# Kernel tuning notes

Measured on AMD Instinct MI355X. Metric: run time of the kernel, lower is better.

## Reference

```python
import jax, jax.numpy as jnp
import numpy as np

N, K, D, E, H = 65536, 8, 256, 256, 132  # points, components, latent_dim, encoder_dim, FC hidden

def setup_inputs() -> dict:
    key = jax.random.key(0)
    ks = jax.random.split(key, 12)
    s = 0.05
    f32 = jnp.float32
    return {
        "signal": jax.random.normal(ks[0], (N, E), f32),
        "components": jax.random.normal(ks[1], (K, N, D), f32),
        # message_map / update_map: Linear(D, D)
        "Wm": jax.random.normal(ks[2], (D, D), f32) * s,
        "bm": jnp.zeros((D,), f32),
        "Wu": jax.random.normal(ks[3], (D, D), f32) * s,
        "bu": jnp.zeros((D,), f32),
        "W0": jax.random.normal(ks[4], (H, E + D), f32) * s,
        "b0": jnp.zeros((H,), f32),
        "W1": jax.random.normal(ks[5], (H, H), f32) * s,
        "b1": jnp.zeros((H,), f32),
        "W2": jax.random.normal(ks[6], (H, H), f32) * s,
        "b2": jnpes if False else jnp.zeros((H,), f32),
        "W3": jax.random.normal(ks[7], (D, H), f32) * s,
        "b3": jnp.zeros((D,), f32),
    }

def reference(signal, components, Wm, bm, Wu, bu, W0, b0, W1, b1, W2, b2, W3, b3):
    k = components.shape[0]
    # sum_k Linear(comp_k) == Linear applied to sum, with bias counted k times (linearity)
    right = components.sum(0) @ Wm.T + k * bm          # [N, D]
    right = right @ Wu.T + bu                          # update_map
    x = jnp.concatenate([signal, right], axis=-1)      # [N, E+D]
    x = jax.nn.relu(x @ W0.T + b0)
    x = jax.nn.relu(x @ W1.T + b1)
    x = jax.nn.relu(x @ W2.T + b2)
    return x @ W3.T + b3                               # [N, D]
```

## Files before the change

### kernel.cpp

```cpp
#include <hip/hip_runtime.h>
#include <hip/hip_bf16.h>


typedef float  f32x4  __attribute__((ext_vector_type(4)));
typedef __bf16 bf16x8 __attribute__((ext_vector_type(8)));
typedef unsigned int   u32x2 __attribute__((ext_vector_type(2)));
typedef unsigned short u16x8 __attribute__((ext_vector_type(8)));

__device__ __forceinline__ unsigned short f2bf(float f) {
  unsigned int u = __builtin_bit_cast(unsigned int, f);
  u += 0x7fffu + ((u >> 16) & 1u);
  return (unsigned short)(u >> 16);
}

__device__ __forceinline__ u32x2 pack4(f32x4 v) {
  u32x2 r;
  r[0] = (unsigned)f2bf(v[0]) | ((unsigned)f2bf(v[1]) << 16);
  r[1] = (unsigned)f2bf(v[2]) | ((unsigned)f2bf(v[3]) << 16);
  return r;
}

__global__ __launch_bounds__(256) void kP(
    const float* __restrict__ W0, const float* __restrict__ Wu,
    const float* __restrict__ Wm, const float* __restrict__ bm,
    const float* __restrict__ bu, const float* __restrict__ b0,
    const float* __restrict__ b1, const float* __restrict__ b2,
    float* __restrict__ Wc, float* __restrict__ bias1,
    float* __restrict__ b1p, float* __restrict__ b2p) {
  const int b = blockIdx.x;
  const int d = threadIdx.x;
  if (b < 132) {
    __shared__ float u[256];
    const int h = b;
    float s = 0.f;
#pragma unroll 8
    for (int i = 0; i < 256; ++i) s += W0[h * 512 + 256 + i] * Wu[i * 256 + d];
    u[d] = s;
    __syncthreads();
    float s2 = 0.f;
#pragma unroll 8
    for (int j = 0; j < 256; ++j) s2 += u[j] * Wm[j * 256 + d];
    Wc[h * 256 + d] = s2;
  } else {
    __shared__ float bml[256];
    __shared__ float rbl[256];
    bml[d] = bm[d];
    __syncthreads();
    {
      const f32x4* wr = (const f32x4*)(Wu + d * 256);
      const f32x4* bm4 = (const f32x4*)bml;
      float s = 0.f;
#pragma unroll 8
      for (int i = 0; i < 64; ++i) {
        f32x4 w = wr[i], v = bm4[i];
        s += w[0] * v[0] + w[1] * v[1] + w[2] * v[2] + w[3] * v[3];
      }
      rbl[d] = 8.f * s + bu[d];
    }
    __syncthreads();
    if (d < 160) {
      float v = 0.f;
      if (d < 132) {
        float s = 0.f;
#pragma unroll 8
        for (int j = 0; j < 256; ++j) s += W0[d * 512 + 256 + j] * rbl[j];
        v = b0[d] + s;
      }
      bias1[d] = v;
      b1p[d] = (d < 132) ? b1[d] : 0.f;
      b2p[d] = (d < 132) ? b2[d] : 0.f;
    }
  }
}

__global__ __launch_bounds__(256) void kC(
    const float* __restrict__ W0, const float* __restrict__ Wc,
    const float* __restrict__ W1, const float* __restrict__ W2,
    const float* __restrict__ W3,
    unsigned short* __restrict__ P1, unsigned short* __restrict__ P2,
    unsigned short* __restrict__ P3, unsigned short* __restrict__ P4) {
  int e = blockIdx.x * 256 + threadIdx.x;
  if (e >= 174080) return;
  unsigned short* dst; int NT, rel, mode;
  if (e < 81920)       { dst = P1; NT = 10; rel = e;          mode = 0; }
  else if (e < 107520) { dst = P2; NT = 10; rel = e - 81920;  mode = 1; }
  else if (e < 133120) { dst = P3; NT = 10; rel = e - 107520; mode = 2; }
  else                 { dst = P4; NT = 16; rel = e - 133120; mode = 3; }
  int chunk = rel >> 9, q = rel & 511;
  int lane = q >> 3, j = q & 7;
  int kk = chunk / NT, nt = chunk - kk * NT;
  int k = kk * 32 + (lane >> 4) * 8 + j;
  int n = nt * 16 + (lane & 15);
  float v = 0.f;
  if (mode == 0) {
    if (n < 132) v = (k < 256) ? W0[n * 512 + k] : Wc[n * 256 + (k - 256)];
  } else if (mode == 1) {
    if (n < 132 && k < 132) v = W1[n * 132 + k];
  } else if (mode == 2) {
    if (n < 132 && k < 132) v = W2[n * 132 + k];
  } else {
    if (k < 132) v = W3[n * 132 + k];
  }
  dst[rel] = f2bf(v);
}

#define WISS(BUF, CHUNK)                                                     \
  {                                                                          \
    _Pragma("unroll") for (int nt = 0; nt < 10; ++nt)                        \
        BUF[nt] = *(const bf16x8*)(Pb + (CHUNK) * 10240 + nt * 1024 +        \
                                   lane * 16);                               \
  }
#define WISS8(BUF, HALF)                                                     \
  {                                                                          \
    _Pragma("unroll") for (int nt = 0; nt < 8; ++nt)                         \
        BUF[nt] = *(const bf16x8*)(Pb + 266240 + (HALF) * 8192 + nt * 1024 + \
                                   lane * 16);                               \
  }
#define MFMA10(BUF)                                                          \
  {                                                                          \
    _Pragma("unroll") for (int nt = 0; nt < 10; ++nt)                        \
        acc[nt] = __builtin_amdgcn_mfma_f32_16x16x32_bf16(af, BUF[nt],       \
                                                          acc[nt], 0, 0, 0); \
  }

__global__ __launch_bounds__(256, 2) void kD(
    const float* __restrict__ signal, const float* __restrict__ comp,
    const unsigned short* __restrict__ Pseq,
    const float* __restrict__ bias1, const float* __restrict__ b1p,
    const float* __restrict__ b2p, const float* __restrict__ b3,
    float* __restrict__ out) {
  extern __shared__ char lds[];
  const int tid = threadIdx.x;
  const int wave = tid >> 6;
  const int lane = tid & 63;
  const int lhalf = lane >> 4;
  const int l16 = lane & 15;
  char* act = lds + wave * 8192;
  const char* Pb = (const char*)Pseq;
  const int row0 = ((int)blockIdx.x * 4 + wave) * 16;
  const int asw = (l16 & 7) << 4;
  const int r2 = lane >> 5, c32 = lane & 31;
  const f32x4* cp = (const f32x4*)comp;
  const size_t cbase = (size_t)(row0 + r2) * 64 + c32 * 2;

  f32x4 sg[16];
  const f32x4* sp = (const f32x4*)signal;
#pragma unroll
  for (int r = 0; r < 16; ++r) sg[r] = sp[(size_t)(row0 + r) * 64 + lane];

  bf16x8 wA[10], wB[10];
  WISS(wA, 0);

  f32x4 ct[4][2];
#pragma unroll
  for (int s = 0; s < 4; ++s) {
    ct[s][0] = cp[cbase + (size_t)s * 4194304u];
    ct[s][1] = cp[cbase + (size_t)s * 4194304u + 1];
  }

#pragma unroll
  for (int r = 0; r < 16; ++r)
    *(u32x2*)(act + r * 512 + ((lane * 8) ^ ((r & 7) << 4))) = pack4(sg[r]);

  f32x4 acc[10];
#pragma unroll
  for (int i = 0; i < 10; ++i) acc[i] = f32x4{0.f, 0.f, 0.f, 0.f};
  f32x4 ca0, ca1;
  u16x8 cs[8];

#pragma unroll
  for (int kk = 0; kk < 8; ++kk) {
    if (kk & 1) { WISS(wA, kk + 1); } else { WISS(wB, kk + 1); }
#pragma unroll
    for (int i = 0; i < 8; ++i) {
      const int s = kk * 8 + i;
      const int b4 = s & 3;
      if (i == 0) { ca0 = ct[b4][0]; ca1 = ct[b4][1]; }
      else        { ca0 += ct[b4][0]; ca1 += ct[b4][1]; }
      if (s + 4 < 64) {
        const int j2 = (s + 4) >> 3, k2 = (s + 4) & 7;
        ct[b4][0] = cp[cbase + (size_t)k2 * 4194304u + j2 * 128];
        ct[b4][1] = cp[cbase + (size_t)k2 * 4194304u + j2 * 128 + 1];
      }
    }
    {
      u16x8 v;
      v[0] = f2bf(ca0[0]); v[1] = f2bf(ca0[1]);
      v[2] = f2bf(ca0[2]); v[3] = f2bf(ca0[3]);
      v[4] = f2bf(ca1[0]); v[5] = f2bf(ca1[1]);
      v[6] = f2bf(ca1[2]); v[7] = f2bf(ca1[3]);
      cs[kk] = v;
    }
    bf16x8 af =
        *(const bf16x8*)(act + l16 * 512 + ((kk * 64 + lhalf * 16) ^ asw));
    if (kk & 1) { MFMA10(wB); } else { MFMA10(wA); }
  }

  asm volatile("" ::: "memory");
#pragma unroll
  for (int j = 0; j < 8; ++j) {
    const int rw = 2 * j + r2;
    *(u16x8*)(act + rw * 512 + ((c32 * 16) ^ ((rw & 7) << 4))) = cs[j];
  }
  asm volatile("" ::: "memory");

#pragma unroll
  for (int kk = 8; kk < 16; ++kk) {
    if (kk & 1) { WISS(wA, kk + 1); } else { WISS(wB, kk + 1); }
    bf16x8 af = *(const bf16x8*)(act + l16 * 512 +
                                 (((kk - 8) * 64 + lhalf * 16) ^ asw));
    if (kk & 1) { MFMA10(wB); } else { MFMA10(wA); }
  }

  {
    float bv[10];
#pragma unroll
    for (int nt = 0; nt < 10; ++nt) bv[nt] = bias1[nt * 16 + l16];
    asm volatile("" ::: "memory");
#pragma unroll
    for (int nt = 0; nt < 10; ++nt) {
#pragma unroll
      for (int r = 0; r < 4; ++r) {
        const int row = lhalf * 4 + r;
        float v = fmaxf(acc[nt][r] + bv[nt], 0.f);
        *(unsigned short*)(act + row * 512 +
                           (((nt * 16 + l16) * 2) ^ ((row & 7) << 4))) = f2bf(v);
      }
    }
    asm volatile("" ::: "memory");
  }

  bf16x8 w4A[8], w4B[8];
#pragma unroll
  for (int L = 0; L < 2; ++L) {
    const float* hbias = L ? b2p : b1p;
#pragma unroll
    for (int i = 0; i < 10; ++i) acc[i] = f32x4{0.f, 0.f, 0.f, 0.f};
#pragma unroll
    for (int q = 0; q < 5; ++q) {
      const int c = 16 + L * 5 + q;
      if (c < 25) {
        if (c & 1) { WISS(wA, c + 1); } else { WISS(wB, c + 1); }
      } else {
        WISS8(w4A, 0);
      }
      bf16x8 af =
          *(const bf16x8*)(act + l16 * 512 + ((q * 64 + lhalf * 16) ^ asw));
      if (c & 1) { MFMA10(wB); } else { MFMA10(wA); }
    }
    float bv[10];
#pragma unroll
    for (int nt = 0; nt < 10; ++nt) bv[nt] = hbias[nt * 16 + l16];
    asm volatile("" ::: "memory");
#pragma unroll
    for (int nt = 0; nt < 10; ++nt) {
#pragma unroll
      for (int r = 0; r < 4; ++r) {
        const int row = lhalf * 4 + r;
        float v = fmaxf(acc[nt][r] + bv[nt], 0.f);
        *(unsigned short*)(act + row * 512 +
                           (((nt * 16 + l16) * 2) ^ ((row & 7) << 4))) = f2bf(v);
      }
    }
    asm volatile("" ::: "memory");
  }

  f32x4 a4[16];
#pragma unroll
  for (int i = 0; i < 16; ++i) a4[i] = f32x4{0.f, 0.f, 0.f, 0.f};
#pragma unroll
  for (int h = 0; h < 10; ++h) {
    if (h < 9) {
      if (h & 1) { WISS8(w4A, h + 1); } else { WISS8(w4B, h + 1); }
    }
    bf16x8 af = *(const bf16x8*)(act + l16 * 512 +
                                 (((h >> 1) * 64 + lhalf * 16) ^ asw));
#pragma unroll
    for (int i = 0; i < 8; ++i) {
      const int nt = (h & 1) * 8 + i;
      if (h & 1)
        a4[nt] = __builtin_amdgcn_mfma_f32_16x16x32_bf16(af, w4B[i], a4[nt],
                                                         0, 0, 0);
      else
        a4[nt] = __builtin_amdgcn_mfma_f32_16x16x32_bf16(af, w4A[i], a4[nt],
                                                         0, 0, 0);
    }
  }

  float bv[16];
#pragma unroll
  for (int nt = 0; nt < 16; ++nt) bv[nt] = b3[nt * 16 + l16];
  float* op = out + (size_t)(row0 + lhalf * 4) * 256 + l16;
#pragma unroll
  for (int nt = 0; nt < 16; ++nt) {
#pragma unroll
    for (int r = 0; r < 4; ++r)
      op[(size_t)r * 256 + nt * 16] = a4[nt][r] + bv[nt];
  }
}

extern "C" void kernel_launch(void* const* d_in, const int* in_sizes, int n_in,
                              void* d_out, int out_size, void* d_ws, size_t ws_size,
                              hipStream_t stream) {
  const float* signal = (const float*)d_in[0];
  const float* comp   = (const float*)d_in[1];
  const float* Wm = (const float*)d_in[2];
  const float* bm = (const float*)d_in[3];
  const float* Wu = (const float*)d_in[4];
  const float* bu = (const float*)d_in[5];
  const float* W0 = (const float*)d_in[6];
  const float* b0 = (const float*)d_in[7];
  const float* W1 = (const float*)d_in[8];
  const float* b1 = (const float*)d_in[9];
  const float* W2 = (const float*)d_in[10];
  const float* b2 = (const float*)d_in[11];
  const float* W3 = (const float*)d_in[12];
  const float* b3 = (const float*)d_in[13];

  char* ws = (char*)d_ws;
  float* Wc    = (float*)(ws + 0);
  float* bias1 = (float*)(ws + 135168);
  float* b1p   = (float*)(ws + 135808);
  float* b2p   = (float*)(ws + 136448);
  unsigned short* P1 = (unsigned short*)(ws + 137216);
  unsigned short* P2 = (unsigned short*)(ws + 301056);
  unsigned short* P3 = (unsigned short*)(ws + 352256);
  unsigned short* P4 = (unsigned short*)(ws + 403456);

  hipLaunchKernelGGL(kP, dim3(133), dim3(256), 0, stream,
                     W0, Wu, Wm, bm, bu, b0, b1, b2, Wc, bias1, b1p, b2p);
  hipLaunchKernelGGL(kC, dim3(680), dim3(256), 0, stream,
                     W0, Wc, W1, W2, W3, P1, P2, P3, P4);
  hipLaunchKernelGGL(kD, dim3(1024), dim3(256), 32768, stream,
                     signal, comp, P1, bias1, b1p, b2p, b3, (float*)d_out);
}
```

Before: 201.4 us.

## Split kernel into producer blocks summing components and consumer MLP blocks with flags

The main kernel now launches 512 blocks. The first 256 blocks stream the components tensor, reduce over K, and write bf16 sums to workspace, then raise per-chunk flags with release atomics. The other 256 blocks each run the MLP over 4 chunks, spin-waiting on those flags before reading the precomputed sums. The aim is to separate the bandwidth-bound reduction from the MFMA work so both run concurrently on different CUs. In exchange it adds an extra write and read of the bf16 sums, and it can deadlock if consumer blocks take all the slots before producer blocks get scheduled.

Result: slower. 800.1 us (+297.3%).

```diff
diff --git a/kernel.cpp b/kernel.cpp
--- a/kernel.cpp
+++ b/kernel.cpp
@@ -26,7 +26,8 @@
     const float* __restrict__ bu, const float* __restrict__ b0,
     const float* __restrict__ b1, const float* __restrict__ b2,
     float* __restrict__ Wc, float* __restrict__ bias1,
-    float* __restrict__ b1p, float* __restrict__ b2p) {
+    float* __restrict__ b1p, float* __restrict__ b2p,
+    int* __restrict__ flags) {
   const int b = blockIdx.x;
   const int d = threadIdx.x;
   if (b < 132) {
@@ -42,6 +43,7 @@
     for (int j = 0; j < 256; ++j) s2 += u[j] * Wm[j * 256 + d];
     Wc[h * 256 + d] = s2;
   } else {
+    flags[d] = 0; flags[d + 256] = 0; flags[d + 512] = 0; flags[d + 768] = 0;
     __shared__ float bml[256];
     __shared__ float rbl[256];
     bml[d] = bm[d];
@@ -123,179 +125,200 @@
                                                           acc[nt], 0, 0, 0); \
   }
 
-__global__ __launch_bounds__(256, 2) void kD(
+__global__ __launch_bounds__(256, 2) void kMain(
     const float* __restrict__ signal, const float* __restrict__ comp,
     const unsigned short* __restrict__ Pseq,
     const float* __restrict__ bias1, const float* __restrict__ b1p,
     const float* __restrict__ b2p, const float* __restrict__ b3,
+    unsigned short* __restrict__ csum, int* flags,
     float* __restrict__ out) {
   extern __shared__ char lds[];
   const int tid = threadIdx.x;
-  const int wave = tid >> 6;
-  const int lane = tid & 63;
-  const int lhalf = lane >> 4;
-  const int l16 = lane & 15;
-  char* act = lds + wave * 8192;
-  const char* Pb = (const char*)Pseq;
-  const int row0 = ((int)blockIdx.x * 4 + wave) * 16;
-  const int asw = (l16 & 7) << 4;
-  const int r2 = lane >> 5, c32 = lane & 31;
-  const f32x4* cp = (const f32x4*)comp;
-  const size_t cbase = (size_t)(row0 + r2) * 64 + c32 * 2;
-
-  f32x4 sg[16];
-  const f32x4* sp = (const f32x4*)signal;
-#pragma unroll
-  for (int r = 0; r < 16; ++r) sg[r] = sp[(size_t)(row0 + r) * 64 + lane];
-
-  bf16x8 wA[10], wB[10];
-  WISS(wA, 0);
-
-  f32x4 ct[4][2];
-#pragma unroll
-  for (int s = 0; s < 4; ++s) {
-    ct[s][0] = cp[cbase + (size_t)s * 4194304u];
-    ct[s][1] = cp[cbase + (size_t)s * 4194304u + 1];
-  }
-
-#pragma unroll
-  for (int r = 0; r < 16; ++r)
-    *(u32x2*)(act + r * 512 + ((lane * 8) ^ ((r & 7) << 4))) = pack4(sg[r]);
-
-  f32x4 acc[10];
-#pragma unroll
-  for (int i = 0; i < 10; ++i) acc[i] = f32x4{0.f, 0.f, 0.f, 0.f};
-  f32x4 ca0, ca1;
-  u16x8 cs[8];
-
-#pragma unroll
-  for (int kk = 0; kk < 8; ++kk) {
-    if (kk & 1) { WISS(wA, kk + 1); } else { WISS(wB, kk + 1); }
-#pragma unroll
-    for (int i = 0; i < 8; ++i) {
-      const int s = kk * 8 + i;
-      const int b4 = s & 3;
-      if (i == 0) { ca0 = ct[b4][0]; ca1 = ct[b4][1]; }
-      else        { ca0 += ct[b4][0]; ca1 += ct[b4][1]; }
-      if (s + 4 < 64) {
-        const int j2 = (s + 4) >> 3, k2 = (s + 4) & 7;
-        ct[b4][0] = cp[cbase + (size_t)k2 * 4194304u + j2 * 128];
-        ct[b4][1] = cp[cbase + (size_t)k2 * 4194304u + j2 * 128 + 1];
+
+  if (blockIdx.x < 256) {
+    const int c = (int)blockIdx.x;
+    const f32x4* cp = (const f32x4*)comp;
+    u32x2* op = (u32x2*)csum;
+    for (int s = 0; s < 4; ++s) {
+      const size_t base = (size_t)(c * 16384 + s * 4096) + tid;
+      f32x4 a[16];
+#pragma unroll
+      for (int j = 0; j < 16; ++j) a[j] = cp[base + j * 256];
+#pragma unroll
+      for (int k = 1; k < 8; ++k) {
+        f32x4 t0[16];
+#pragma unroll
+        for (int j = 0; j < 16; ++j)
+          t0[j] = cp[base + (size_t)k * 4194304u + j * 256];
+#pragma unroll
+        for (int j = 0; j < 16; ++j) a[j] += t0[j];
+      }
+#pragma unroll
+      for (int j = 0; j < 16; ++j) op[base + j * 256] = pack4(a[j]);
+      __syncthreads();
+      if (tid == 0) {
+        __threadfence();
+        __hip_atomic_store(&flags[c * 4 + s], 1, __ATOMIC_RELEASE,
+                           __HIP_MEMORY_SCOPE_AGENT);
       }
     }
-    {
-      u16x8 v;
-      v[0] = f2bf(ca0[0]); v[1] = f2bf(ca0[1]);
-      v[2] = f2bf(ca0[2]); v[3] = f2bf(ca0[3]);
-      v[4] = f2bf(ca1[0]); v[5] = f2bf(ca1[1]);
-      v[6] = f2bf(ca1[2]); v[7] = f2bf(ca1[3]);
-      cs[kk] = v;
+  } else {
+    const int c = (int)blockIdx.x - 256;
+    const int wave = tid >> 6;
+    const int lane = tid & 63;
+    const int lhalf = lane >> 4;
+    const int l16 = lane & 15;
+    const int r2 = lane >> 5, c32 = lane & 31;
+    char* act = lds + wave * 8192;
+    const char* Pb = (const char*)Pseq;
+    const int asw = (l16 & 7) << 4;
+
+    for (int s = 0; s < 4; ++s) {
+      const int row0 = c * 256 + s * 64 + wave * 16;
+
+      {
+        f32x4 sg[16];
+        const f32x4* sp = (const f32x4*)signal;
+#pragma unroll
+        for (int r = 0; r < 16; ++r) sg[r] = sp[(size_t)(row0 + r) * 64 + lane];
+#pragma unroll
+        for (int r = 0; r < 16; ++r)
+          *(u32x2*)(act + r * 512 + ((lane * 8) ^ ((r & 7) << 4))) =
+              pack4(sg[r]);
+      }
+
+      bf16x8 wA[10], wB[10];
+      WISS(wA, 0);
+
+      {
+        const int fi = c * 4 + s;
+        while (__hip_atomic_load(&flags[fi], __ATOMIC_ACQUIRE,
+                                 __HIP_MEMORY_SCOPE_AGENT) == 0)
+          __builtin_amdgcn_s_sleep(16);
+      }
+
+      u16x8 cs[8];
+#pragma unroll
+      for (int j = 0; j < 8; ++j)
+        cs[j] = *(const u16x8*)(csum + (size_t)(row0 + 2 * j + r2) * 256 +
+                                c32 * 8);
+
+      f32x4 acc[10];
+#pragma unroll
+      for (int i = 0; i < 10; ++i) acc[i] = f32x4{0.f, 0.f, 0.f, 0.f};
+
+#pragma unroll
+      for (int kk = 0; kk < 8; ++kk) {
+        if (kk & 1) { WISS(wA, kk + 1); } else { WISS(wB, kk + 1); }
+        bf16x8 af =
+            *(const bf16x8*)(act + l16 * 512 + ((kk * 64 + lhalf * 16) ^ asw));
+        if (kk & 1) { MFMA10(wB); } else { MFMA10(wA); }
+      }
+
+      asm volatile("" ::: "memory");
+#pragma unroll
+      for (int j = 0; j < 8; ++j) {
+        const int rw = 2 * j + r2;
+        *(u16x8*)(act + rw * 512 + ((c32 * 16) ^ ((rw & 7) << 4))) = cs[j];
+      }
+      asm volatile("" ::: "memory");
+
+#pragma unroll
+      for (int kk = 8; kk < 16; ++kk) {
+        if (kk & 1) { WISS(wA, kk + 1); } else { WISS(wB, kk + 1); }
+        bf16x8 af = *(const bf16x8*)(act + l16 * 512 +
+                                     (((kk - 8) * 64 + lhalf * 16) ^ asw));
+        if (kk & 1) { MFMA10(wB); } else { MFMA10(wA); }
+      }
+
+      {
+        float bv[10];
+#pragma unroll
+        for (int nt = 0; nt < 10; ++nt) bv[nt] = bias1[nt * 16 + l16];
+        asm volatile("" ::: "memory");
+#pragma unroll
+        for (int nt = 0; nt < 10; ++nt) {
+#pragma unroll
+          for (int r = 0; r < 4; ++r) {
+            const int row = lhalf * 4 + r;
+            float v = fmaxf(acc[nt][r] + bv[nt], 0.f);
+            *(unsigned short*)(act + row * 512 +
+                               (((nt * 16 + l16) * 2) ^ ((row & 7) << 4))) =
+                f2bf(v);
+          }
+        }
+        asm volatile("" ::: "memory");
+      }
+
+      bf16x8 w4A[8], w4B[8];
+#pragma unroll
+      for (int L = 0; L < 2; ++L) {
+        const float* hbias = L ? b2p : b1p;
+#pragma unroll
+        for (int i = 0; i < 10; ++i) acc[i] = f32x4{0.f, 0.f, 0.f, 0.f};
+#pragma unroll
+        for (int q = 0; q < 5; ++q) {
+          const int cc = 16 + L * 5 + q;
+          if (cc < 25) {
+            if (cc & 1) { WISS(wA, cc + 1); } else { WISS(wB, cc + 1); }
+          } else {
+            WISS8(w4A, 0);
+          }
+          bf16x8 af =
+              *(const bf16x8*)(act + l16 * 512 + ((q * 64 + lhalf * 16) ^ asw));
+          if (cc & 1) { MFMA10(wB); } else { MFMA10(wA); }
+        }
+        float bv[10];
+#pragma unroll
+        for (int nt = 0; nt < 10; ++nt) bv[nt] = hbias[nt * 16 + l16];
+        asm volatile("" ::: "memory");
+#pragma unroll
+        for (int nt = 0; nt < 10; ++nt) {
+#pragma unroll
+          for (int r = 0; r < 4; ++r) {
+            const int row = lhalf * 4 + r;
+            float v = fmaxf(acc[nt][r] + bv[nt], 0.f);
+            *(unsigned short*)(act + row * 512 +
+                               (((nt * 16 + l16) * 2) ^ ((row & 7) << 4))) =
+                f2bf(v);
+          }
+        }
+        asm volatile("" ::: "memory");
+      }
+
+      f32x4 a4[16];
+#pragma unroll
+      for (int i = 0; i < 16; ++i) a4[i] = f32x4{0.f, 0.f, 0.f, 0.f};
+#pragma unroll
+      for (int h = 0; h < 10; ++h) {
+        if (h < 9) {
+          if (h & 1) { WISS8(w4A, h + 1); } else { WISS8(w4B, h + 1); }
+        }
+        bf16x8 af = *(const bf16x8*)(act + l16 * 512 +
+                                     (((h >> 1) * 64 + lhalf * 16) ^ asw));
+#pragma unroll
+        for (int i = 0; i < 8; ++i) {
+          const int nt = (h & 1) * 8 + i;
+          if (h & 1)
+            a4[nt] = __builtin_amdgcn_mfma_f32_16x16x32_bf16(af, w4B[i],
+                                                             a4[nt], 0, 0, 0);
+          else
+            a4[nt] = __builtin_amdgcn_mfma_f32_16x16x32_bf16(af, w4A[i],
+                                                             a4[nt], 0, 0, 0);
+        }
+      }
+
+      float bv[16];
+#pragma unroll
+      for (int nt = 0; nt < 16; ++nt) bv[nt] = b3[nt * 16 + l16];
+      float* op = out + (size_t)(row0 + lhalf * 4) * 256 + l16;
+#pragma unroll
+      for (int nt = 0; nt < 16; ++nt) {
+#pragma unroll
+        for (int r = 0; r < 4; ++r)
+          op[(size_t)r * 256 + nt * 16] = a4[nt][r] + bv[nt];
+      }
     }
-    bf16x8 af =
-        *(const bf16x8*)(act + l16 * 512 + ((kk * 64 + lhalf * 16) ^ asw));
-    if (kk & 1) { MFMA10(wB); } else { MFMA10(wA); }
-  }
-
-  asm volatile("" ::: "memory");
-#pragma unroll
-  for (int j = 0; j < 8; ++j) {
-    const int rw = 2 * j + r2;
-    *(u16x8*)(act + rw * 512 + ((c32 * 16) ^ ((rw & 7) << 4))) = cs[j];
-  }
-  asm volatile("" ::: "memory");
-
-#pragma unroll
-  for (int kk = 8; kk < 16; ++kk) {
-    if (kk & 1) { WISS(wA, kk + 1); } else { WISS(wB, kk + 1); }
-    bf16x8 af = *(const bf16x8*)(act + l16 * 512 +
-                                 (((kk - 8) * 64 + lhalf * 16) ^ asw));
-    if (kk & 1) { MFMA10(wB); } else { MFMA10(wA); }
-  }
-
-  {
-    float bv[10];
-#pragma unroll
-    for (int nt = 0; nt < 10; ++nt) bv[nt] = bias1[nt * 16 + l16];
-    asm volatile("" ::: "memory");
-#pragma unroll
-    for (int nt = 0; nt < 10; ++nt) {
-#pragma unroll
-      for (int r = 0; r < 4; ++r) {
-        const int row = lhalf * 4 + r;
-        float v = fmaxf(acc[nt][r] + bv[nt], 0.f);
-        *(unsigned short*)(act + row * 512 +
-                           (((nt * 16 + l16) * 2) ^ ((row & 7) << 4))) = f2bf(v);
-      }
-    }
-    asm volatile("" ::: "memory");
-  }
-
-  bf16x8 w4A[8], w4B[8];
-#pragma unroll
-  for (int L = 0; L < 2; ++L) {
-    const float* hbias = L ? b2p : b1p;
-#pragma unroll
-    for (int i = 0; i < 10; ++i) acc[i] = f32x4{0.f, 0.f, 0.f, 0.f};
-#pragma unroll
-    for (int q = 0; q < 5; ++q) {
-      const int c = 16 + L * 5 + q;
-      if (c < 25) {
-        if (c & 1) { WISS(wA, c + 1); } else { WISS(wB, c + 1); }
-      } else {
-        WISS8(w4A, 0);
-      }
-      bf16x8 af =
-          *(const bf16x8*)(act + l16 * 512 + ((q * 64 + lhalf * 16) ^ asw));
-      if (c & 1) { MFMA10(wB); } else { MFMA10(wA); }
-    }
-    float bv[10];
-#pragma unroll
-    for (int nt = 0; nt < 10; ++nt) bv[nt] = hbias[nt * 16 + l16];
-    asm volatile("" ::: "memory");
-#pragma unroll
-    for (int nt = 0; nt < 10; ++nt) {
-#pragma unroll
-      for (int r = 0; r < 4; ++r) {
-        const int row = lhalf * 4 + r;
-        float v = fmaxf(acc[nt][r] + bv[nt], 0.f);
-        *(unsigned short*)(act + row * 512 +
-                           (((nt * 16 + l16) * 2) ^ ((row & 7) << 4))) = f2bf(v);
-      }
-    }
-    asm volatile("" ::: "memory");
-  }
-
-  f32x4 a4[16];
-#pragma unroll
-  for (int i = 0; i < 16; ++i) a4[i] = f32x4{0.f, 0.f, 0.f, 0.f};
-#pragma unroll
-  for (int h = 0; h < 10; ++h) {
-    if (h < 9) {
-      if (h & 1) { WISS8(w4A, h + 1); } else { WISS8(w4B, h + 1); }
-    }
-    bf16x8 af = *(const bf16x8*)(act + l16 * 512 +
-                                 (((h >> 1) * 64 + lhalf * 16) ^ asw));
-#pragma unroll
-    for (int i = 0; i < 8; ++i) {
-      const int nt = (h & 1) * 8 + i;
-      if (h & 1)
-        a4[nt] = __builtin_amdgcn_mfma_f32_16x16x32_bf16(af, w4B[i], a4[nt],
-                                                         0, 0, 0);
-      else
-        a4[nt] = __builtin_amdgcn_mfma_f32_16x16x32_bf16(af, w4A[i], a4[nt],
-                                                         0, 0, 0);
-    }
-  }
-
-  float bv[16];
-#pragma unroll
-  for (int nt = 0; nt < 16; ++nt) bv[nt] = b3[nt * 16 + l16];
-  float* op = out + (size_t)(row0 + lhalf * 4) * 256 + l16;
-#pragma unroll
-  for (int nt = 0; nt < 16; ++nt) {
-#pragma unroll
-    for (int r = 0; r < 4; ++r)
-      op[(size_t)r * 256 + nt * 16] = a4[nt][r] + bv[nt];
   }
 }
 
@@ -326,11 +349,15 @@
   unsigned short* P2 = (unsigned short*)(ws + 301056);
   unsigned short* P3 = (unsigned short*)(ws + 352256);
   unsigned short* P4 = (unsigned short*)(ws + 403456);
+  int* flags = (int*)(ws + 485376);
+  unsigned short* csum = (unsigned short*)(ws + 489472);
 
   hipLaunchKernelGGL(kP, dim3(133), dim3(256), 0, stream,
-                     W0, Wu, Wm, bm, bu, b0, b1, b2, Wc, bias1, b1p, b2p);
+                     W0, Wu, Wm, bm, bu, b0, b1, b2, Wc, bias1, b1p, b2p,
+                     flags);
   hipLaunchKernelGGL(kC, dim3(680), dim3(256), 0, stream,
                      W0, Wc, W1, W2, W3, P1, P2, P3, P4);
-  hipLaunchKernelGGL(kD, dim3(1024), dim3(256), 32768, stream,
-                     signal, comp, P1, bias1, b1p, b2p, b3, (float*)d_out);
-}
+  hipLaunchKernelGGL(kMain, dim3(512), dim3(256), 32768, stream,
+                     signal, comp, P1, bias1, b1p, b2p, b3, csum, flags,
+                     (float*)d_out);
+}
```

## Feed first-layer MFMA directly from global loads without component pre-summing

Applied to the files above, without the earlier changes.

The first layer no longer sums the K components in registers and stages signal and summed components through LDS. Each lane now loads its MFMA A-fragment straight from global memory, converts it with the hardware packed bf16 convert instruction, and runs one MFMA per component chunk. This relies on the folded weight being the same for every component, so the summation happens inside the MFMA accumulation. That removes the LDS write/read round trip and the manual rounding code, but it multiplies first-layer MFMA work about 5x (72 instead of 16 k-steps) and issues smaller strided global loads.

Measured after the change: 273.0 us. +35.6%, slower.

```diff
diff --git a/kernel.cpp b/kernel.cpp
--- a/kernel.cpp
+++ b/kernel.cpp
@@ -4,8 +4,7 @@
 
 typedef float  f32x4  __attribute__((ext_vector_type(4)));
 typedef __bf16 bf16x8 __attribute__((ext_vector_type(8)));
-typedef unsigned int   u32x2 __attribute__((ext_vector_type(2)));
-typedef unsigned short u16x8 __attribute__((ext_vector_type(8)));
+typedef unsigned int   u32x4 __attribute__((ext_vector_type(4)));
 
 __device__ __forceinline__ unsigned short f2bf(float f) {
   unsigned int u = __builtin_bit_cast(unsigned int, f);
@@ -13,11 +12,14 @@
   return (unsigned short)(u >> 16);
 }
 
-__device__ __forceinline__ u32x2 pack4(f32x4 v) {
-  u32x2 r;
-  r[0] = (unsigned)f2bf(v[0]) | ((unsigned)f2bf(v[1]) << 16);
-  r[1] = (unsigned)f2bf(v[2]) | ((unsigned)f2bf(v[3]) << 16);
-  return r;
+__device__ __forceinline__ bf16x8 cvt8(f32x4 a, f32x4 b) {
+  unsigned r0, r1, r2, r3;
+  asm("v_cvt_pk_bf16_f32 %0, %1, %2" : "=v"(r0) : "v"(a[0]), "v"(a[1]));
+  asm("v_cvt_pk_bf16_f32 %0, %1, %2" : "=v"(r1) : "v"(a[2]), "v"(a[3]));
+  asm("v_cvt_pk_bf16_f32 %0, %1, %2" : "=v"(r2) : "v"(b[0]), "v"(b[1]));
+  asm("v_cvt_pk_bf16_f32 %0, %1, %2" : "=v"(r3) : "v"(b[2]), "v"(b[3]));
+  u32x4 r{r0, r1, r2, r3};
+  return __builtin_bit_cast(bf16x8, r);
 }
 
 __global__ __launch_bounds__(256) void kP(
@@ -139,77 +141,44 @@
   const char* Pb = (const char*)Pseq;
   const int row0 = ((int)blockIdx.x * 4 + wave) * 16;
   const int asw = (l16 & 7) << 4;
-  const int r2 = lane >> 5, c32 = lane & 31;
+
+  const f32x4* sp = (const f32x4*)signal;
   const f32x4* cp = (const f32x4*)comp;
-  const size_t cbase = (size_t)(row0 + r2) * 64 + c32 * 2;
-
-  f32x4 sg[16];
-  const f32x4* sp = (const f32x4*)signal;
-#pragma unroll
-  for (int r = 0; r < 16; ++r) sg[r] = sp[(size_t)(row0 + r) * 64 + lane];
+  const size_t abase = (size_t)(row0 + l16) * 64 + lhalf * 2;
 
   bf16x8 wA[10], wB[10];
   WISS(wA, 0);
 
-  f32x4 ct[4][2];
-#pragma unroll
-  for (int s = 0; s < 4; ++s) {
-    ct[s][0] = cp[cbase + (size_t)s * 4194304u];
-    ct[s][1] = cp[cbase + (size_t)s * 4194304u + 1];
-  }
-
-#pragma unroll
-  for (int r = 0; r < 16; ++r)
-    *(u32x2*)(act + r * 512 + ((lane * 8) ^ ((r & 7) << 4))) = pack4(sg[r]);
+  f32x4 c0 = sp[abase], c1 = sp[abase + 1];
+  f32x4 n0, n1;
 
   f32x4 acc[10];
 #pragma unroll
   for (int i = 0; i < 10; ++i) acc[i] = f32x4{0.f, 0.f, 0.f, 0.f};
-  f32x4 ca0, ca1;
-  u16x8 cs[8];
-
-#pragma unroll
-  for (int kk = 0; kk < 8; ++kk) {
-    if (kk & 1) { WISS(wA, kk + 1); } else { WISS(wB, kk + 1); }
-#pragma unroll
-    for (int i = 0; i < 8; ++i) {
-      const int s = kk * 8 + i;
-      const int b4 = s & 3;
-      if (i == 0) { ca0 = ct[b4][0]; ca1 = ct[b4][1]; }
-      else        { ca0 += ct[b4][0]; ca1 += ct[b4][1]; }
-      if (s + 4 < 64) {
-        const int j2 = (s + 4) >> 3, k2 = (s + 4) & 7;
-        ct[b4][0] = cp[cbase + (size_t)k2 * 4194304u + j2 * 128];
-        ct[b4][1] = cp[cbase + (size_t)k2 * 4194304u + j2 * 128 + 1];
-      }
-    }
-    {
-      u16x8 v;
-      v[0] = f2bf(ca0[0]); v[1] = f2bf(ca0[1]);
-      v[2] = f2bf(ca0[2]); v[3] = f2bf(ca0[3]);
-      v[4] = f2bf(ca1[0]); v[5] = f2bf(ca1[1]);
-      v[6] = f2bf(ca1[2]); v[7] = f2bf(ca1[3]);
-      cs[kk] = v;
-    }
-    bf16x8 af =
-        *(const bf16x8*)(act + l16 * 512 + ((kk * 64 + lhalf * 16) ^ asw));
-    if (kk & 1) { MFMA10(wB); } else { MFMA10(wA); }
-  }
-
-  asm volatile("" ::: "memory");
-#pragma unroll
-  for (int j = 0; j < 8; ++j) {
-    const int rw = 2 * j + r2;
-    *(u16x8*)(act + rw * 512 + ((c32 * 16) ^ ((rw & 7) << 4))) = cs[j];
-  }
-  asm volatile("" ::: "memory");
-
-#pragma unroll
-  for (int kk = 8; kk < 16; ++kk) {
-    if (kk & 1) { WISS(wA, kk + 1); } else { WISS(wB, kk + 1); }
-    bf16x8 af = *(const bf16x8*)(act + l16 * 512 +
-                                 (((kk - 8) * 64 + lhalf * 16) ^ asw));
-    if (kk & 1) { MFMA10(wB); } else { MFMA10(wA); }
+
+#pragma unroll
+  for (int p = 0; p < 72; ++p) {
+    if (p < 8) {
+      const int cn = p + 1;
+      if (cn & 1) { WISS(wB, cn); } else { WISS(wA, cn); }
+    } else if (((p - 8) & 7) == 0 && p >= 8) {
+      const int cn = 9 + ((p - 8) >> 3);
+      if (cn & 1) { WISS(wB, cn); } else { WISS(wA, cn); }
+    }
+    if (p + 1 < 8) {
+      n0 = sp[abase + (size_t)(p + 1) * 8];
+      n1 = sp[abase + (size_t)(p + 1) * 8 + 1];
+    } else if (p + 1 < 72) {
+      const int q = p + 1 - 8, kkq = q >> 3, kq = q & 7;
+      const size_t ci = (size_t)kq * 4194304u + abase + (size_t)kkq * 8;
+      n0 = cp[ci];
+      n1 = cp[ci + 1];
+    }
+    bf16x8 af = cvt8(c0, c1);
+    const int cur = (p < 8) ? p : (8 + ((p - 8) >> 3));
+    if (cur & 1) { MFMA10(wB); } else { MFMA10(wA); }
+    c0 = n0;
+    c1 = n1;
   }
 
   {
@@ -237,16 +206,16 @@
 #pragma unroll
     for (int i = 0; i < 10; ++i) acc[i] = f32x4{0.f, 0.f, 0.f, 0.f};
 #pragma unroll
-    for (int q = 0; q < 5; ++q) {
-      const int c = 16 + L * 5 + q;
-      if (c < 25) {
-        if (c & 1) { WISS(wA, c + 1); } else { WISS(wB, c + 1); }
+    for (int qq = 0; qq < 5; ++qq) {
+      const int cc = 16 + L * 5 + qq;
+      if (cc < 25) {
+        if (cc & 1) { WISS(wA, cc + 1); } else { WISS(wB, cc + 1); }
       } else {
         WISS8(w4A, 0);
       }
       bf16x8 af =
-          *(const bf16x8*)(act + l16 * 512 + ((q * 64 + lhalf * 16) ^ asw));
-      if (c & 1) { MFMA10(wB); } else { MFMA10(wA); }
+          *(const bf16x8*)(act + l16 * 512 + ((qq * 64 + lhalf * 16) ^ asw));
+      if (cc & 1) { MFMA10(wB); } else { MFMA10(wA); }
     }
     float bv[10];
 #pragma unroll
```

## Process two row tiles per wave, prefetching next tile's components during MLP

Applied to the files above, without the earlier changes.

Each wave now handles two 16-row tiles instead of one, with half the blocks launched. The strided component loads and sums for the second tile are issued in stages across the first tile's MLP phases, so that HBM latency overlaps with MFMA work. The component half of the first layer is also moved ahead of the signal half. The W3 stage is split into two 128-column halves to lower register pressure. The cost is fewer waves in flight and heavier register use from the pending prefetch buffers, which could cause spills or reduce latency hiding.

Result: slower. 344.4 us (+71.0%).

```diff
diff --git a/kernel.cpp b/kernel.cpp
--- a/kernel.cpp
+++ b/kernel.cpp
@@ -5,6 +5,7 @@
 typedef float  f32x4  __attribute__((ext_vector_type(4)));
 typedef __bf16 bf16x8 __attribute__((ext_vector_type(8)));
 typedef unsigned int   u32x2 __attribute__((ext_vector_type(2)));
+typedef unsigned int   u32x4 __attribute__((ext_vector_type(4)));
 typedef unsigned short u16x8 __attribute__((ext_vector_type(8)));
 
 __device__ __forceinline__ unsigned short f2bf(float f) {
@@ -110,20 +111,70 @@
         BUF[nt] = *(const bf16x8*)(Pb + (CHUNK) * 10240 + nt * 1024 +        \
                                    lane * 16);                               \
   }
-#define WISS8(BUF, HALF)                                                     \
+#define WISS8L4(BUF, Q)                                                      \
   {                                                                          \
     _Pragma("unroll") for (int nt = 0; nt < 8; ++nt)                         \
-        BUF[nt] = *(const bf16x8*)(Pb + 266240 + (HALF) * 8192 + nt * 1024 + \
-                                   lane * 16);                               \
-  }
-#define MFMA10(BUF)                                                          \
+        BUF[nt] = *(const bf16x8*)(Pb + 266240 + ((Q) % 5) * 16384 +         \
+                                   ((Q) / 5) * 8192 + nt * 1024 + lane * 16);\
+  }
+#define MFMA10(ACC, BUF, AF)                                                 \
   {                                                                          \
     _Pragma("unroll") for (int nt = 0; nt < 10; ++nt)                        \
-        acc[nt] = __builtin_amdgcn_mfma_f32_16x16x32_bf16(af, BUF[nt],       \
-                                                          acc[nt], 0, 0, 0); \
-  }
-
-__global__ __launch_bounds__(256, 2) void kD(
+        ACC[nt] = __builtin_amdgcn_mfma_f32_16x16x32_bf16(AF, BUF[nt],       \
+                                                          ACC[nt], 0, 0, 0); \
+  }
+
+__device__ constexpr int SS(int f) {
+  return (f <= 0) ? 0 : (f < 8 ? 3 * f : (f < 28 ? 24 + 2 * (f - 8) : 64));
+}
+#define SCONSUME(PHI)                                                        \
+  {                                                                          \
+    _Pragma("unroll") for (int pi = SS((PHI) - 2); pi < SS((PHI) - 1); ++pi){\
+      csa[pi >> 3] += pend[pi % 6][0];                                       \
+      csb[pi >> 3] += pend[pi % 6][1];                                       \
+    }                                                                        \
+  }
+#define SISSUE(PHI)                                                          \
+  {                                                                          \
+    _Pragma("unroll") for (int pi = SS(PHI); pi < SS((PHI) + 1); ++pi) {     \
+      const size_t ci = (size_t)(pi & 7) * 4194304u + nbase +                \
+                        (size_t)(pi >> 3) * 128;                             \
+      pend[pi % 6][0] = cp[ci];                                              \
+      pend[pi % 6][1] = cp[ci + 1];                                          \
+    }                                                                        \
+  }
+#define SSTEP(PHI) { SCONSUME(PHI); SISSUE(PHI); }
+
+#define WCS()                                                                \
+  {                                                                          \
+    asm volatile("" ::: "memory");                                           \
+    _Pragma("unroll") for (int j = 0; j < 8; ++j) {                          \
+      const int rw = 2 * j + r2;                                             \
+      u32x2 lo = pack4(csa[j]), hi = pack4(csb[j]);                          \
+      *(u32x4*)(act + rw * 512 + ((c32 * 16) ^ ((rw & 7) << 4))) =           \
+          u32x4{lo[0], lo[1], hi[0], hi[1]};                                 \
+    }                                                                        \
+    asm volatile("" ::: "memory");                                           \
+  }
+#define BIASRELU(BIASP)                                                      \
+  {                                                                          \
+    float bv[10];                                                            \
+    _Pragma("unroll") for (int nt = 0; nt < 10; ++nt)                        \
+        bv[nt] = (BIASP)[nt * 16 + l16];                                     \
+    asm volatile("" ::: "memory");                                           \
+    _Pragma("unroll") for (int nt = 0; nt < 10; ++nt) {                      \
+      _Pragma("unroll") for (int r = 0; r < 4; ++r) {                        \
+        const int row = lhalf * 4 + r;                                       \
+        float v = fmaxf(acc[nt][r] + bv[nt], 0.f);                           \
+        *(unsigned short*)(act + row * 512 +                                 \
+                           (((nt * 16 + l16) * 2) ^ ((row & 7) << 4))) =     \
+            f2bf(v);                                                         \
+      }                                                                      \
+    }                                                                        \
+    asm volatile("" ::: "memory");                                           \
+  }
+
+__global__ __launch_bounds__(256, 2) void kF(
     const float* __restrict__ signal, const float* __restrict__ comp,
     const unsigned short* __restrict__ Pseq,
     const float* __restrict__ bias1, const float* __restrict__ b1p,
@@ -135,167 +186,220 @@
   const int lane = tid & 63;
   const int lhalf = lane >> 4;
   const int l16 = lane & 15;
+  const int r2 = lane >> 5, c32 = lane & 31;
   char* act = lds + wave * 8192;
   const char* Pb = (const char*)Pseq;
-  const int row0 = ((int)blockIdx.x * 4 + wave) * 16;
+  const int gid = (int)blockIdx.x * 4 + wave;
+  const int row0 = gid * 32;
+  const int row1 = row0 + 16;
   const int asw = (l16 & 7) << 4;
-  const int r2 = lane >> 5, c32 = lane & 31;
+  const f32x4* sp = (const f32x4*)signal;
   const f32x4* cp = (const f32x4*)comp;
-  const size_t cbase = (size_t)(row0 + r2) * 64 + c32 * 2;
-
+  const size_t base0 = (size_t)(row0 + r2) * 64 + c32 * 2;
+  const size_t nbase = (size_t)(row1 + r2) * 64 + c32 * 2;
+
+  bf16x8 wA[10], wB[10], w4A[8], w4B[8];
+  f32x4 csa[8], csb[8], pend[6][2];
+  f32x4 acc[10];
   f32x4 sg[16];
-  const f32x4* sp = (const f32x4*)signal;
+
+  WISS(wA, 8);
 #pragma unroll
   for (int r = 0; r < 16; ++r) sg[r] = sp[(size_t)(row0 + r) * 64 + lane];
-
-  bf16x8 wA[10], wB[10];
-  WISS(wA, 0);
-
-  f32x4 ct[4][2];
-#pragma unroll
-  for (int s = 0; s < 4; ++s) {
-    ct[s][0] = cp[cbase + (size_t)s * 4194304u];
-    ct[s][1] = cp[cbase + (size_t)s * 4194304u + 1];
-  }
-
+#pragma unroll
+  for (int j = 0; j < 8; ++j) {
+    csa[j] = f32x4{0.f, 0.f, 0.f, 0.f};
+    csb[j] = f32x4{0.f, 0.f, 0.f, 0.f};
+  }
+#pragma unroll
+  for (int pi = 0; pi < 70; ++pi) {
+    if (pi >= 6) {
+      const int q = pi - 6;
+      csa[q >> 3] += pend[q % 6][0];
+      csb[q >> 3] += pend[q % 6][1];
+    }
+    if (pi < 64) {
+      const size_t ci =
+          (size_t)(pi & 7) * 4194304u + base0 + (size_t)(pi >> 3) * 128;
+      pend[pi % 6][0] = cp[ci];
+      pend[pi % 6][1] = cp[ci + 1];
+    }
+  }
+  WCS();
+#pragma unroll
+  for (int j = 0; j < 8; ++j) {
+    csa[j] = f32x4{0.f, 0.f, 0.f, 0.f};
+    csb[j] = f32x4{0.f, 0.f, 0.f, 0.f};
+  }
+
+#pragma unroll
+  for (int i = 0; i < 10; ++i) acc[i] = f32x4{0.f, 0.f, 0.f, 0.f};
+#pragma unroll
+  for (int ph = 0; ph < 8; ++ph) {
+    const int cn = (ph < 7) ? (9 + ph) : 0;
+    if ((ph + 1) & 1) { WISS(wB, cn); } else { WISS(wA, cn); }
+    bf16x8 af =
+        *(const bf16x8*)(act + l16 * 512 + ((ph * 64 + lhalf * 16) ^ asw));
+    if (ph & 1) { MFMA10(acc, wB, af); } else { MFMA10(acc, wA, af); }
+  }
+  asm volatile("" ::: "memory");
 #pragma unroll
   for (int r = 0; r < 16; ++r)
     *(u32x2*)(act + r * 512 + ((lane * 8) ^ ((r & 7) << 4))) = pack4(sg[r]);
-
-  f32x4 acc[10];
-#pragma unroll
-  for (int i = 0; i < 10; ++i) acc[i] = f32x4{0.f, 0.f, 0.f, 0.f};
-  f32x4 ca0, ca1;
-  u16x8 cs[8];
-
-#pragma unroll
-  for (int kk = 0; kk < 8; ++kk) {
-    if (kk & 1) { WISS(wA, kk + 1); } else { WISS(wB, kk + 1); }
-#pragma unroll
-    for (int i = 0; i < 8; ++i) {
-      const int s = kk * 8 + i;
-      const int b4 = s & 3;
-      if (i == 0) { ca0 = ct[b4][0]; ca1 = ct[b4][1]; }
-      else        { ca0 += ct[b4][0]; ca1 += ct[b4][1]; }
-      if (s + 4 < 64) {
-        const int j2 = (s + 4) >> 3, k2 = (s + 4) & 7;
-        ct[b4][0] = cp[cbase + (size_t)k2 * 4194304u + j2 * 128];
-        ct[b4][1] = cp[cbase + (size_t)k2 * 4194304u + j2 * 128 + 1];
-      }
-    }
-    {
-      u16x8 v;
-      v[0] = f2bf(ca0[0]); v[1] = f2bf(ca0[1]);
-      v[2] = f2bf(ca0[2]); v[3] = f2bf(ca0[3]);
-      v[4] = f2bf(ca1[0]); v[5] = f2bf(ca1[1]);
-      v[6] = f2bf(ca1[2]); v[7] = f2bf(ca1[3]);
-      cs[kk] = v;
-    }
+  asm volatile("" ::: "memory");
+#pragma unroll
+  for (int ph = 8; ph < 16; ++ph) {
+    const int f = ph - 8;
+    SSTEP(f);
+    const int cn = (ph < 15) ? (f + 1) : 16;
+    if ((ph + 1) & 1) { WISS(wB, cn); } else { WISS(wA, cn); }
     bf16x8 af =
-        *(const bf16x8*)(act + l16 * 512 + ((kk * 64 + lhalf * 16) ^ asw));
-    if (kk & 1) { MFMA10(wB); } else { MFMA10(wA); }
-  }
-
-  asm volatile("" ::: "memory");
-#pragma unroll
-  for (int j = 0; j < 8; ++j) {
-    const int rw = 2 * j + r2;
-    *(u16x8*)(act + rw * 512 + ((c32 * 16) ^ ((rw & 7) << 4))) = cs[j];
-  }
-  asm volatile("" ::: "memory");
-
-#pragma unroll
-  for (int kk = 8; kk < 16; ++kk) {
-    if (kk & 1) { WISS(wA, kk + 1); } else { WISS(wB, kk + 1); }
-    bf16x8 af = *(const bf16x8*)(act + l16 * 512 +
-                                 (((kk - 8) * 64 + lhalf * 16) ^ asw));
-    if (kk & 1) { MFMA10(wB); } else { MFMA10(wA); }
-  }
-
-  {
-    float bv[10];
-#pragma unroll
-    for (int nt = 0; nt < 10; ++nt) bv[nt] = bias1[nt * 16 + l16];
-    asm volatile("" ::: "memory");
-#pragma unroll
-    for (int nt = 0; nt < 10; ++nt) {
-#pragma unroll
-      for (int r = 0; r < 4; ++r) {
-        const int row = lhalf * 4 + r;
-        float v = fmaxf(acc[nt][r] + bv[nt], 0.f);
-        *(unsigned short*)(act + row * 512 +
-                           (((nt * 16 + l16) * 2) ^ ((row & 7) << 4))) = f2bf(v);
-      }
-    }
-    asm volatile("" ::: "memory");
-  }
-
-  bf16x8 w4A[8], w4B[8];
+        *(const bf16x8*)(act + l16 * 512 + ((f * 64 + lhalf * 16) ^ asw));
+    if (ph & 1) { MFMA10(acc, wB, af); } else { MFMA10(acc, wA, af); }
+  }
+  BIASRELU(bias1);
 #pragma unroll
   for (int L = 0; L < 2; ++L) {
-    const float* hbias = L ? b2p : b1p;
 #pragma unroll
     for (int i = 0; i < 10; ++i) acc[i] = f32x4{0.f, 0.f, 0.f, 0.f};
 #pragma unroll
     for (int q = 0; q < 5; ++q) {
-      const int c = 16 + L * 5 + q;
-      if (c < 25) {
-        if (c & 1) { WISS(wA, c + 1); } else { WISS(wB, c + 1); }
+      const int ph = 16 + L * 5 + q;
+      const int f = ph - 8;
+      const int cc = 16 + L * 5 + q;
+      SSTEP(f);
+      if (cc < 25) {
+        if ((ph + 1) & 1) { WISS(wB, cc + 1); } else { WISS(wA, cc + 1); }
       } else {
-        WISS8(w4A, 0);
+        WISS8L4(w4A, 0);
       }
       bf16x8 af =
           *(const bf16x8*)(act + l16 * 512 + ((q * 64 + lhalf * 16) ^ asw));
-      if (c & 1) { MFMA10(wB); } else { MFMA10(wA); }
-    }
-    float bv[10];
-#pragma unroll
-    for (int nt = 0; nt < 10; ++nt) bv[nt] = hbias[nt * 16 + l16];
-    asm volatile("" ::: "memory");
-#pragma unroll
-    for (int nt = 0; nt < 10; ++nt) {
-#pragma unroll
-      for (int r = 0; r < 4; ++r) {
-        const int row = lhalf * 4 + r;
-        float v = fmaxf(acc[nt][r] + bv[nt], 0.f);
-        *(unsigned short*)(act + row * 512 +
-                           (((nt * 16 + l16) * 2) ^ ((row & 7) << 4))) = f2bf(v);
-      }
-    }
-    asm volatile("" ::: "memory");
-  }
-
-  f32x4 a4[16];
-#pragma unroll
-  for (int i = 0; i < 16; ++i) a4[i] = f32x4{0.f, 0.f, 0.f, 0.f};
-#pragma unroll
-  for (int h = 0; h < 10; ++h) {
-    if (h < 9) {
-      if (h & 1) { WISS8(w4A, h + 1); } else { WISS8(w4B, h + 1); }
-    }
-    bf16x8 af = *(const bf16x8*)(act + l16 * 512 +
-                                 (((h >> 1) * 64 + lhalf * 16) ^ asw));
+      if (ph & 1) { MFMA10(acc, wB, af); } else { MFMA10(acc, wA, af); }
+    }
+    if (L) { BIASRELU(b2p); } else { BIASRELU(b1p); }
+  }
+#pragma unroll
+  for (int H = 0; H < 2; ++H) {
+    f32x4 a4[8];
+#pragma unroll
+    for (int i = 0; i < 8; ++i) a4[i] = f32x4{0.f, 0.f, 0.f, 0.f};
+#pragma unroll
+    for (int kk = 0; kk < 5; ++kk) {
+      const int q = H * 5 + kk;
+      const int f = 18 + q;
+      SSTEP(f);
+      if (q < 9) {
+        if (q & 1) { WISS8L4(w4A, q + 1); } else { WISS8L4(w4B, q + 1); }
+      } else {
+        WISS(wA, 8);
+      }
+      bf16x8 af =
+          *(const bf16x8*)(act + l16 * 512 + ((kk * 64 + lhalf * 16) ^ asw));
+#pragma unroll
+      for (int i = 0; i < 8; ++i) {
+        if (q & 1)
+          a4[i] = __builtin_amdgcn_mfma_f32_16x16x32_bf16(af, w4B[i], a4[i],
+                                                          0, 0, 0);
+        else
+          a4[i] = __builtin_amdgcn_mfma_f32_16x16x32_bf16(af, w4A[i], a4[i],
+                                                          0, 0, 0);
+      }
+    }
+    float bv[8];
+#pragma unroll
+    for (int i = 0; i < 8; ++i) bv[i] = b3[(H * 8 + i) * 16 + l16];
+    float* op = out + (size_t)(row0 + lhalf * 4) * 256 + H * 128 + l16;
 #pragma unroll
     for (int i = 0; i < 8; ++i) {
-      const int nt = (h & 1) * 8 + i;
-      if (h & 1)
-        a4[nt] = __builtin_amdgcn_mfma_f32_16x16x32_bf16(af, w4B[i], a4[nt],
-                                                         0, 0, 0);
-      else
-        a4[nt] = __builtin_amdgcn_mfma_f32_16x16x32_bf16(af, w4A[i], a4[nt],
-                                                         0, 0, 0);
-    }
-  }
-
-  float bv[16];
-#pragma unroll
-  for (int nt = 0; nt < 16; ++nt) bv[nt] = b3[nt * 16 + l16];
-  float* op = out + (size_t)(row0 + lhalf * 4) * 256 + l16;
-#pragma unroll
-  for (int nt = 0; nt < 16; ++nt) {
-#pragma unroll
-    for (int r = 0; r < 4; ++r)
-      op[(size_t)r * 256 + nt * 16] = a4[nt][r] + bv[nt];
+#pragma unroll
+      for (int r = 0; r < 4; ++r)
+        op[(size_t)r * 256 + i * 16] = a4[i][r] + bv[i];
+    }
+  }
+  SCONSUME(28);
+  SCONSUME(29);
+
+  WCS();
+#pragma unroll
+  for (int i = 0; i < 10; ++i) acc[i] = f32x4{0.f, 0.f, 0.f, 0.f};
+#pragma unroll
+  for (int ph = 0; ph < 8; ++ph) {
+    sg[2 * ph] = sp[(size_t)(row1 + 2 * ph) * 64 + lane];
+    sg[2 * ph + 1] = sp[(size_t)(row1 + 2 * ph + 1) * 64 + lane];
+    const int cn = (ph < 7) ? (9 + ph) : 0;
+    if ((ph + 1) & 1) { WISS(wB, cn); } else { WISS(wA, cn); }
+    bf16x8 af =
+        *(const bf16x8*)(act + l16 * 512 + ((ph * 64 + lhalf * 16) ^ asw));
+    if (ph & 1) { MFMA10(acc, wB, af); } else { MFMA10(acc, wA, af); }
+  }
+  asm volatile("" ::: "memory");
+#pragma unroll
+  for (int r = 0; r < 16; ++r)
+    *(u32x2*)(act + r * 512 + ((lane * 8) ^ ((r & 7) << 4))) = pack4(sg[r]);
+  asm volatile("" ::: "memory");
+#pragma unroll
+  for (int ph = 8; ph < 16; ++ph) {
+    const int f = ph - 8;
+    const int cn = (ph < 15) ? (f + 1) : 16;
+    if ((ph + 1) & 1) { WISS(wB, cn); } else { WISS(wA, cn); }
+    bf16x8 af =
+        *(const bf16x8*)(act + l16 * 512 + ((f * 64 + lhalf * 16) ^ asw));
+    if (ph & 1) { MFMA10(acc, wB, af); } else { MFMA10(acc, wA, af); }
+  }
+  BIASRELU(bias1);
+#pragma unroll
+  for (int L = 0; L < 2; ++L) {
+#pragma unroll
+    for (int i = 0; i < 10; ++i) acc[i] = f32x4{0.f, 0.f, 0.f, 0.f};
+#pragma unroll
+    for (int q = 0; q < 5; ++q) {
+      const int ph = 16 + L * 5 + q;
+      const int cc = 16 + L * 5 + q;
+      if (cc < 25) {
+        if ((ph + 1) & 1) { WISS(wB, cc + 1); } else { WISS(wA, cc + 1); }
+      } else {
+        WISS8L4(w4A, 0);
+      }
+      bf16x8 af =
+          *(const bf16x8*)(act + l16 * 512 + ((q * 64 + lhalf * 16) ^ asw));
+      if (ph & 1) { MFMA10(acc, wB, af); } else { MFMA10(acc, wA, af); }
+    }
+    if (L) { BIASRELU(b2p); } else { BIASRELU(b1p); }
+  }
+#pragma unroll
+  for (int H = 0; H < 2; ++H) {
+    f32x4 a4[8];
+#pragma unroll
+    for (int i = 0; i < 8; ++i) a4[i] = f32x4{0.f, 0.f, 0.f, 0.f};
+#pragma unroll
+    for (int kk = 0; kk < 5; ++kk) {
+      const int q = H * 5 + kk;
+      if (q < 9) {
+        if (q & 1) { WISS8L4(w4A, q + 1); } else { WISS8L4(w4B, q + 1); }
+      }
+      bf16x8 af =
+          *(const bf16x8*)(act + l16 * 512 + ((kk * 64 + lhalf * 16) ^ asw));
+#pragma unroll
+      for (int i = 0; i < 8; ++i) {
+        if (q & 1)
+          a4[i] = __builtin_amdgcn_mfma_f32_16x16x32_bf16(af, w4B[i], a4[i],
+                                                          0, 0, 0);
+        else
+          a4[i] = __builtin_amdgcn_mfma_f32_16x16x32_bf16(af, w4A[i], a4[i],
+                                                          0, 0, 0);
+      }
+    }
+    float bv[8];
+#pragma unroll
+    for (int i = 0; i < 8; ++i) bv[i] = b3[(H * 8 + i) * 16 + l16];
+    float* op = out + (size_t)(row1 + lhalf * 4) * 256 + H * 128 + l16;
+#pragma unroll
+    for (int i = 0; i < 8; ++i) {
+#pragma unroll
+      for (int r = 0; r < 4; ++r)
+        op[(size_t)r * 256 + i * 16] = a4[i][r] + bv[i];
+    }
   }
 }
 
@@ -331,6 +435,6 @@
                      W0, Wu, Wm, bm, bu, b0, b1, b2, Wc, bias1, b1p, b2p);
   hipLaunchKernelGGL(kC, dim3(680), dim3(256), 0, stream,
                      W0, Wc, W1, W2, W3, P1, P2, P3, P4);
-  hipLaunchKernelGGL(kD, dim3(1024), dim3(256), 32768, stream,
+  hipLaunchKernelGGL(kF, dim3(512), dim3(256), 32768, stream,
                      signal, comp, P1, bias1, b1p, b2p, b3, (float*)d_out);
 }
```
